# Kernel tuning notes

Measured on AMD Instinct MI355X. Metric: run time of the kernel, lower is better.

Reference implementation:

```python
import jax, jax.numpy as jnp
import numpy as np

D_MODEL = 1024
N_HEAD = 16
HEAD_DIM = D_MODEL // N_HEAD
ROPE_BASE = 10000.0


def _weight_quant(w):
    # BitNet b1.58 ternary weight quant with per-tensor absmean scale (STE).
    scale = jnp.clip(jnp.mean(jnp.abs(w)), 1e-5, None)
    wq = jnp.clip(jnp.round(w / scale), -1.0, 1.0) * scale
    return w + jax.lax.stop_gradient(wq - w)


def _act_quant(x):
    # Per-token int8 absmax activation quant (STE).
    scale = 127.0 / jnp.clip(jnp.max(jnp.abs(x), axis=-1, keepdims=True), 1e-5, None)
    xq = jnp.clip(jnp.round(x * scale), -128.0, 127.0) / scale
    return x + jax.lax.stop_gradient(xq - x)


def _bitlinear(x, w):
    # y = act_quant(x) @ weight_quant(w).T   (torch Linear convention, no bias)
    return _act_quant(x) @ _weight_quant(w).T


def _rope(x, pos):
    # x: [B, H, T, D]; half-split rotation.
    d = x.shape[-1]
    inv_freq = 1.0 / (ROPE_BASE ** (jnp.arange(0, d, 2, dtype=jnp.float32) / d))
    ang = pos[:, None].astype(jnp.float32) * inv_freq[None, :]  # [T, D/2]
    cos, sin = jnp.cos(ang), jnp.sin(ang)
    x1, x2 = x[..., : d // 2], x[..., d // 2 :]
    return jnp.concatenate([x1 * cos - x2 * sin, x1 * sin + x2 * cos], axis=-1)


def setup_inputs() -> dict:
    key = jax.random.key(0)
    k0, k1, k2, k3, k4 = jax.random.split(key, 5)
    B, T = 2, 2048
    s = 1.0 / np.sqrt(D_MODEL)
    return {
        "x": jax.random.normal(k0, (B, T, D_MODEL), dtype=jnp.float32),
        "Wq": jax.random.normal(k1, (D_MODEL, D_MODEL), dtype=jnp.float32) * s,
        "Wk": jax.random.normal(k2, (D_MODEL, D_MODEL), dtype=jnp.float32) * s,
        "Wv": jax.random.normal(k3, (D_MODEL, D_MODEL), dtype=jnp.float32) * s,
        "Wo": jax.random.normal(k4, (D_MODEL, D_MODEL), dtype=jnp.float32) * s,
    }


def reference(x, Wq, Wk, Wv, Wo):
    B, T, C = x.shape
    pos = jnp.arange(T)
    def heads(y):
        return y.reshape(B, T, N_HEAD, HEAD_DIM).transpose(0, 2, 1, 3)  # [B,H,T,D]
    q = _rope(heads(_bitlinear(x, Wq)), pos)
    k = _rope(heads(_bitlinear(x, Wk)), pos)
    v = heads(_bitlinear(x, Wv))
    scores = jnp.einsum("bhqd,bhkd->bhqk", q, k) / jnp.sqrt(jnp.float32(HEAD_DIM))
    causal = jnp.tril(jnp.ones((T, T), dtype=bool))
    scores = jnp.where(causal[None, None], scores, jnp.finfo(scores.dtype).min)
    att = jax.nn.softmax(scores, axis=-1)
    y = jnp.einsum("bhqk,bhkd->bhqd", att, v)  # [B,H,T,D]
    y = y.transpose(0, 2, 1, 3).reshape(B, T, C)
    return _bitlinear(y, Wo)
```

## Files before the change

### kernel.cpp

```cpp
#include <hip/hip_runtime.h>
#include <hip/hip_bf16.h>
#include <math.h>

typedef __bf16 bf16_t;
typedef signed char i8_t;
typedef __attribute__((ext_vector_type(8))) __bf16 bf16x8;
typedef __attribute__((ext_vector_type(4))) __bf16 bf16x4;
typedef __attribute__((ext_vector_type(4))) float f32x4;
typedef __attribute__((ext_vector_type(4))) int i32x4;

typedef __attribute__((address_space(3))) void lds_void_t;
typedef const __attribute__((address_space(1))) void glb_void_t;
#define GLOAD_LDS(g, l) __builtin_amdgcn_global_load_lds((glb_void_t*)(g), (lds_void_t*)(l), 16, 0, 0)

#define MFMA16(a,b,c) __builtin_amdgcn_mfma_f32_16x16x32_bf16(a,b,c,0,0,0)
#define MFMAI8(a,b,c) __builtin_amdgcn_mfma_i32_16x16x64_i8(a,b,c,0,0,0)

#if __has_builtin(__builtin_amdgcn_exp2f)
#define EXP2F(x) __builtin_amdgcn_exp2f(x)
#else
#define EXP2F(x) exp2f(x)
#endif

static constexpr int TSEQ = 2048;
static constexpr int CDIM = 1024;
#define NEG_BIG (-1.0e30f)
#define Q_PRESCALE 0.18033688011112042f
#define ROPE_C 0.41524101190971284f

__global__ __launch_bounds__(256) void wreduce(const float* __restrict__ W0, const float* __restrict__ W1,
                                               const float* __restrict__ W2, const float* __restrict__ W3,
                                               double* __restrict__ partial) {
  int w = blockIdx.x >> 6, b = blockIdx.x & 63;
  const float* W = (w==0)?W0:(w==1)?W1:(w==2)?W2:W3;
  const float* base = W + (size_t)b * 16384;
  double s = 0.0;
  for (int i = threadIdx.x * 4; i < 16384; i += 1024) {
    float4 v = *(const float4*)(base + i);
    s += (double)fabsf(v.x) + (double)fabsf(v.y) + (double)fabsf(v.z) + (double)fabsf(v.w);
  }
  #pragma unroll
  for (int off = 1; off < 64; off <<= 1) s += __shfl_xor(s, off);
  __shared__ double red[4];
  if ((threadIdx.x & 63) == 0) red[threadIdx.x >> 6] = s;
  __syncthreads();
  if (threadIdx.x == 0) partial[blockIdx.x] = red[0] + red[1] + red[2] + red[3];
}

__global__ __launch_bounds__(256) void prep(const float* __restrict__ W0, const float* __restrict__ W1,
                                            const float* __restrict__ W2, const float* __restrict__ W3,
                                            const double* __restrict__ partial, float* __restrict__ wscale,
                                            i8_t* __restrict__ wq_all,
                                            const float* __restrict__ xg, i8_t* __restrict__ xqg,
                                            float* __restrict__ rowfac, float2* __restrict__ ropetab) {
  int bid = blockIdx.x;
  if (bid < 4096) {
    int w = bid >> 10;
    double ssum = 0.0;
    for (int i = 0; i < 64; ++i) ssum += partial[w * 64 + i];
    float s = fmaxf((float)(ssum * (1.0 / 1048576.0)), 1e-5f);
    if ((bid & 1023) == 0 && threadIdx.x == 0) wscale[w] = s;
    const float* W = (w==0)?W0:(w==1)?W1:(w==2)?W2:W3;
    int off = ((bid & 1023) * 256 + threadIdx.x) * 4;
    float4 v = *(const float4*)(W + off);
    char4 q;
    q.x = (i8_t)(int)fminf(fmaxf(rintf(v.x / s), -1.f), 1.f);
    q.y = (i8_t)(int)fminf(fmaxf(rintf(v.y / s), -1.f), 1.f);
    q.z = (i8_t)(int)fminf(fmaxf(rintf(v.z / s), -1.f), 1.f);
    q.w = (i8_t)(int)fminf(fmaxf(rintf(v.w / s), -1.f), 1.f);
    *(char4*)(wq_all + (size_t)w * 1048576 + off) = q;
  } else if (bid < 8192) {
    int r = bid - 4096;
    float4 v = *(const float4*)(xg + (size_t)r * 1024 + threadIdx.x * 4);
    float mx = fmaxf(fmaxf(fabsf(v.x), fabsf(v.y)), fmaxf(fabsf(v.z), fabsf(v.w)));
    #pragma unroll
    for (int off = 1; off < 64; off <<= 1) mx = fmaxf(mx, __shfl_xor(mx, off));
    __shared__ float red[4];
    if ((threadIdx.x & 63) == 0) red[threadIdx.x >> 6] = mx;
    __syncthreads();
    mx = fmaxf(fmaxf(red[0], red[1]), fmaxf(red[2], red[3]));
    mx = fmaxf(mx, 1e-5f);
    float scale = 127.0f / mx;
    if (threadIdx.x == 0) rowfac[r] = mx * (1.0f / 127.0f);
    char4 q;
    q.x = (i8_t)(int)fminf(fmaxf(rintf(v.x * scale), -128.f), 127.f);
    q.y = (i8_t)(int)fminf(fmaxf(rintf(v.y * scale), -128.f), 127.f);
    q.z = (i8_t)(int)fminf(fmaxf(rintf(v.z * scale), -128.f), 127.f);
    q.w = (i8_t)(int)fminf(fmaxf(rintf(v.w * scale), -128.f), 127.f);
    *(char4*)(xqg + (size_t)r * 1024 + threadIdx.x * 4) = q;
  } else {
    int t = (bid - 8192) * 8 + (threadIdx.x >> 5);
    int ii = threadIdx.x & 31;
    float ang = (float)t * exp2f(-(float)ii * ROPE_C);
    float sn, cs;
    sincosf(ang, &sn, &cs);
    ropetab[t * 32 + ii] = make_float2(cs, sn);
  }
}

__global__ __launch_bounds__(256) void actquant(const float* __restrict__ yf0, const float* __restrict__ yf1,
                                                const float* __restrict__ den0, const float* __restrict__ den1,
                                                i8_t* __restrict__ xqg, float* __restrict__ rowfac) {
  int r = blockIdx.x;
  int b = r >> 11, t = r & 2047;
  int h = threadIdx.x >> 4;
  size_t idx = (size_t)r * 1024 + threadIdx.x * 4;
  float4 v0 = *(const float4*)(yf0 + idx);
  float4 v1 = *(const float4*)(yf1 + idx);
  size_t di = (size_t)(b * 16 + h) * 2048 + t;
  float inv = 1.0f / (den0[di] + den1[di]);
  float4 v;
  v.x = (v0.x + v1.x) * inv;
  v.y = (v0.y + v1.y) * inv;
  v.z = (v0.z + v1.z) * inv;
  v.w = (v0.w + v1.w) * inv;
  float mx = fmaxf(fmaxf(fabsf(v.x), fabsf(v.y)), fmaxf(fabsf(v.z), fabsf(v.w)));
  #pragma unroll
  for (int off = 1; off < 64; off <<= 1) mx = fmaxf(mx, __shfl_xor(mx, off));
  __shared__ float red[4];
  if ((threadIdx.x & 63) == 0) red[threadIdx.x >> 6] = mx;
  __syncthreads();
  mx = fmaxf(fmaxf(red[0], red[1]), fmaxf(red[2], red[3]));
  mx = fmaxf(mx, 1e-5f);
  float scale = 127.0f / mx;
  if (threadIdx.x == 0) rowfac[r] = mx * (1.0f / 127.0f);
  char4 q;
  q.x = (i8_t)(int)fminf(fmaxf(rintf(v.x * scale), -128.f), 127.f);
  q.y = (i8_t)(int)fminf(fmaxf(rintf(v.y * scale), -128.f), 127.f);
  q.z = (i8_t)(int)fminf(fmaxf(rintf(v.z * scale), -128.f), 127.f);
  q.w = (i8_t)(int)fminf(fmaxf(rintf(v.w * scale), -128.f), 127.f);
  *(char4*)(xqg + (size_t)r * 1024 + threadIdx.x * 4) = q;
}

__global__ __launch_bounds__(256) void gemm_qkv(const i8_t* __restrict__ xq, const i8_t* __restrict__ wq_all,
                                                const float* __restrict__ wscale, const float* __restrict__ rowfac,
                                                const float2* __restrict__ ropetab,
                                                bf16_t* __restrict__ qb, bf16_t* __restrict__ kb,
                                                bf16_t* __restrict__ vtb) {
  const int z = blockIdx.z;
  const i8_t* Bw = wq_all + (size_t)z * 1048576;
  const int m0 = blockIdx.x * 128, n0 = blockIdx.y * 128;
  const int tid = threadIdx.x;
  const int wave = tid >> 6, lane = tid & 63, quad = lane >> 4, l16 = lane & 15;
  const int wm = wave >> 1, wn = wave & 1;
  __shared__ __align__(16) i8_t As[2][128 * 64];
  __shared__ __align__(16) i8_t Bs[2][128 * 64];
  i32x4 zero = {0, 0, 0, 0};
  i32x4 acc[4][4];
  #pragma unroll
  for (int i = 0; i < 4; ++i)
    #pragma unroll
    for (int j = 0; j < 4; ++j) acc[i][j] = zero;

  const int row_s = tid >> 2;
  const int cg16 = (((tid & 3) - (row_s >> 1)) & 3) * 16;
  const int sw16 = ((quad + (l16 >> 1)) & 3) * 16;

  #pragma unroll
  for (int v2 = 0; v2 < 2; ++v2) {
    int v = tid + v2 * 256;
    int row = row_s + v2 * 64;
    GLOAD_LDS(&xq[(size_t)(m0 + row) * 1024 + cg16], &As[0][v * 16]);
    GLOAD_LDS(&Bw[(size_t)(n0 + row) * 1024 + cg16], &Bs[0][v * 16]);
  }
  __syncthreads();

  #pragma unroll 2
  for (int kt = 0; kt < 16; ++kt) {
    const int cur = kt & 1;
    if (kt < 15) {
      #pragma unroll
      for (int v2 = 0; v2 < 2; ++v2) {
        int v = tid + v2 * 256;
        int row = row_s + v2 * 64;
        GLOAD_LDS(&xq[(size_t)(m0 + row) * 1024 + (kt + 1) * 64 + cg16], &As[cur ^ 1][v * 16]);
        GLOAD_LDS(&Bw[(size_t)(n0 + row) * 1024 + (kt + 1) * 64 + cg16], &Bs[cur ^ 1][v * 16]);
      }
    }
    i32x4 af[4], bfr[4];
    #pragma unroll
    for (int i = 0; i < 4; ++i) af[i] = *(const i32x4*)&As[cur][(wm * 64 + i * 16 + l16) * 64 + sw16];
    #pragma unroll
    for (int j = 0; j < 4; ++j) bfr[j] = *(const i32x4*)&Bs[cur][(wn * 64 + j * 16 + l16) * 64 + sw16];
    if (z == 2) {
      #pragma unroll
      for (int i = 0; i < 4; ++i)
        #pragma unroll
        for (int j = 0; j < 4; ++j) acc[i][j] = MFMAI8(bfr[i], af[j], acc[i][j]);
    } else {
      #pragma unroll
      for (int i = 0; i < 4; ++i)
        #pragma unroll
        for (int j = 0; j < 4; ++j) acc[i][j] = MFMAI8(af[i], bfr[j], acc[i][j]);
    }
    __syncthreads();
  }
  float ws = wscale[z] * (z == 0 ? Q_PRESCALE : 1.0f);
  if (z <= 1) {
    bf16_t* dst = (z == 0) ? qb : kb;
    const int h = (n0 >> 6) + wn;
    #pragma unroll
    for (int i = 0; i < 4; ++i) {
      #pragma unroll
      for (int r = 0; r < 4; ++r) {
        int m = m0 + wm * 64 + i * 16 + quad * 4 + r;
        float rf = rowfac[m] * ws;
        int b = m >> 11, t = m & 2047;
        bf16_t* drow = dst + (((size_t)b * 16 + h) * 2048 + t) * 64;
        #pragma unroll
        for (int j = 0; j < 2; ++j) {
          int dd1 = j * 16 + l16;
          float2 cs2 = ropetab[t * 32 + dd1];
          float v1 = (float)acc[i][j][r] * rf;
          float v2 = (float)acc[i][j + 2][r] * rf;
          drow[dd1]      = (bf16_t)(v1 * cs2.x - v2 * cs2.y);
          drow[dd1 + 32] = (bf16_t)(v1 * cs2.y + v2 * cs2.x);
        }
      }
    }
  } else {
    const int b = m0 >> 11;
    const int tbase = (m0 & 2047) + wm * 64;
    float rfj[4];
    #pragma unroll
    for (int j = 0; j < 4; ++j) rfj[j] = rowfac[m0 + wm * 64 + j * 16 + l16] * ws;
    #pragma unroll
    for (int i = 0; i < 4; ++i) {
      #pragma unroll
      for (int r = 0; r < 4; ++r) {
        int nrow = n0 + wn * 64 + i * 16 + quad * 4 + r;
        int h = nrow >> 6, dd = nrow & 63;
        bf16_t* vrow = vtb + (((size_t)b * 16 + h) * 64 + dd) * 2048 + tbase;
        #pragma unroll
        for (int j = 0; j < 4; ++j) vrow[j * 16 + l16] = (bf16_t)((float)acc[i][j][r] * rfj[j]);
      }
    }
  }
}

__global__ __launch_bounds__(256) void gemm_out(const i8_t* __restrict__ yq, const i8_t* __restrict__ wo,
                                                const float* __restrict__ wscale, const float* __restrict__ rowfac,
                                                float* __restrict__ out) {
  const int m0 = blockIdx.x * 128, n0 = blockIdx.y * 128;
  const int tid = threadIdx.x;
  const int wave = tid >> 6, lane = tid & 63, quad = lane >> 4, l16 = lane & 15;
  const int wm = wave >> 1, wn = wave & 1;
  __shared__ __align__(16) i8_t As[2][128 * 64];
  __shared__ __align__(16) i8_t Bs[2][128 * 64];
  i32x4 zero = {0, 0, 0, 0};
  i32x4 acc[4][4];
  #pragma unroll
  for (int i = 0; i < 4; ++i)
    #pragma unroll
    for (int j = 0; j < 4; ++j) acc[i][j] = zero;

  const int row_s = tid >> 2;
  const int cg16 = (((tid & 3) - (row_s >> 1)) & 3) * 16;
  const int sw16 = ((quad + (l16 >> 1)) & 3) * 16;

  #pragma unroll
  for (int v2 = 0; v2 < 2; ++v2) {
    int v = tid + v2 * 256;
    int row = row_s + v2 * 64;
    GLOAD_LDS(&yq[(size_t)(m0 + row) * 1024 + cg16], &As[0][v * 16]);
    GLOAD_LDS(&wo[(size_t)(n0 + row) * 1024 + cg16], &Bs[0][v * 16]);
  }
  __syncthreads();

  #pragma unroll 2
  for (int kt = 0; kt < 16; ++kt) {
    const int cur = kt & 1;
    if (kt < 15) {
      #pragma unroll
      for (int v2 = 0; v2 < 2; ++v2) {
        int v = tid + v2 * 256;
        int row = row_s + v2 * 64;
        GLOAD_LDS(&yq[(size_t)(m0 + row) * 1024 + (kt + 1) * 64 + cg16], &As[cur ^ 1][v * 16]);
        GLOAD_LDS(&wo[(size_t)(n0 + row) * 1024 + (kt + 1) * 64 + cg16], &Bs[cur ^ 1][v * 16]);
      }
    }
    i32x4 af[4], bfr[4];
    #pragma unroll
    for (int i = 0; i < 4; ++i) af[i] = *(const i32x4*)&As[cur][(wm * 64 + i * 16 + l16) * 64 + sw16];
    #pragma unroll
    for (int j = 0; j < 4; ++j) bfr[j] = *(const i32x4*)&Bs[cur][(wn * 64 + j * 16 + l16) * 64 + sw16];
    #pragma unroll
    for (int i = 0; i < 4; ++i)
      #pragma unroll
      for (int j = 0; j < 4; ++j) acc[i][j] = MFMAI8(af[i], bfr[j], acc[i][j]);
    __syncthreads();
  }
  float ws = wscale[3];
  #pragma unroll
  for (int i = 0; i < 4; ++i) {
    #pragma unroll
    for (int r = 0; r < 4; ++r) {
      int m = m0 + wm * 64 + i * 16 + quad * 4 + r;
      float rf = rowfac[m] * ws;
      #pragma unroll
      for (int j = 0; j < 4; ++j) {
        int n = n0 + wn * 64 + j * 16 + l16;
        out[(size_t)m * 1024 + n] = (float)acc[i][j][r] * rf;
      }
    }
  }
}

__global__ __launch_bounds__(512) void flash_attn(const bf16_t* __restrict__ qg, const bf16_t* __restrict__ kg,
                                                  const bf16_t* __restrict__ vtg,
                                                  float* __restrict__ yf0, float* __restrict__ yf1,
                                                  float* __restrict__ den0, float* __restrict__ den1) {
  const int lid = (int)blockIdx.y * 8 + (int)blockIdx.x;
  const int par = (lid >> 3) & 1;
  const int p   = (lid >> 4) & 7;
  const int bh  = (lid & 7) * 4 + (lid >> 7);
  float* __restrict__ yo = par ? yf1 : yf0;
  float* __restrict__ dn = par ? den1 : den0;
  const int tid = threadIdx.x;
  const int wave = tid >> 6, lane = tid & 63;
  const int quad = lane >> 4, l16 = lane & 15;

  __shared__ __align__(16) bf16_t Kb[2][64 * 64];
  __shared__ __align__(16) bf16_t Vb[2][64 * 64];
  __shared__ __align__(16) bf16_t Pl[8][16 * 72];

  const int b = bh >> 4, h = bh & 15;
  bf16_t* Pw = &Pl[wave][0];

  const int r0 = tid >> 3, cblk = tid & 7;
  const int ldsOff0 = r0 * 64 + ((cblk ^ (r0 & 7)) * 8);
  const size_t bhbase = (size_t)bh * 131072;
  const bf16_t* kbase0 = kg + bhbase + r0 * 64 + cblk * 8;
  const bf16_t* vbase0 = vtg + bhbase + r0 * 2048 + cblk * 8;

  int kf_off[4][2];
  #pragma unroll
  for (int n = 0; n < 4; ++n)
    #pragma unroll
    for (int c = 0; c < 2; ++c)
      kf_off[n][c] = (n * 16 + l16) * 64 + (((c * 4 + quad) ^ (l16 & 7)) * 8);

  bf16x8 ones;
  #pragma unroll
  for (int j = 0; j < 8; ++j) ones[j] = (bf16_t)1.0f;
  f32x4 zero = {0.f, 0.f, 0.f, 0.f};

  bf16x8 kpre = *(const bf16x8*)(kbase0 + par * 4096);
  bf16x8 vpre = *(const bf16x8*)(vbase0 + par * 64);

  int cum = 0;
  #pragma unroll 1
  for (int tsel = 0; tsel < 2; ++tsel) {
    const int qt = tsel ? (15 - p) : p;
    const int kcmax = 2 * qt + 1;
    const int qbw = qt * 128 + wave * 16;

    const bf16_t* qrowp = qg + ((size_t)bh * TSEQ + qbw + l16) * 64;
    bf16x8 aq0 = *(const bf16x8*)(qrowp + quad * 8);
    bf16x8 aq1 = *(const bf16x8*)(qrowp + 32 + quad * 8);

    f32x4 o[4], o5;
    #pragma unroll
    for (int i = 0; i < 4; ++i) o[i] = zero;
    o5 = zero;

    #pragma unroll 1
    for (int kc = par; kc <= kcmax; kc += 2, ++cum) {
      const int buf = cum & 1;
      bf16_t* Kt = &Kb[buf][0];
      bf16_t* Vt = &Vb[buf][0];
      *(bf16x8*)&Kt[ldsOff0] = kpre;
      *(bf16x8*)&Vt[ldsOff0] = vpre;
      __syncthreads();
      int nkc = (kc + 2 <= kcmax) ? (kc + 2) : ((tsel == 0) ? par : -1);
      if (nkc >= 0) {
        kpre = *(const bf16x8*)(kbase0 + nkc * 4096);
        vpre = *(const bf16x8*)(vbase0 + nkc * 64);
      }

      if (kc * 64 > qbw + 15) continue;

      f32x4 s[4];
      __builtin_amdgcn_s_setprio(1);
      #pragma unroll
      for (int n = 0; n < 4; ++n) {
        bf16x8 bk0 = *(const bf16x8*)&Kt[kf_off[n][0]];
        bf16x8 bk1 = *(const bf16x8*)&Kt[kf_off[n][1]];
        s[n] = MFMA16(aq1, bk1, MFMA16(aq0, bk0, zero));
      }
      __builtin_amdgcn_s_setprio(0);
      if (kc * 64 + 63 > qbw) {
        #pragma unroll
        for (int n = 0; n < 4; ++n)
          #pragma unroll
          for (int r = 0; r < 4; ++r) {
            int kpos = kc * 64 + n * 16 + l16;
            int qpos = qbw + quad * 4 + r;
            if (kpos > qpos) s[n][r] = NEG_BIG;
          }
      }
      #pragma unroll
      for (int n = 0; n < 4; ++n)
        #pragma unroll
        for (int r = 0; r < 4; ++r)
          Pw[(quad * 4 + r) * 72 + n * 16 + l16] = (bf16_t)EXP2F(s[n][r]);

      bf16x8 ap0 = *(const bf16x8*)&Pw[l16 * 72 + quad * 8];
      bf16x8 ap1 = *(const bf16x8*)&Pw[l16 * 72 + 32 + quad * 8];
      __builtin_amdgcn_s_setprio(1);
      #pragma unroll
      for (int nh = 0; nh < 4; ++nh) {
        bf16x8 bv0 = *(const bf16x8*)&Vt[kf_off[nh][0]];
        bf16x8 bv1 = *(const bf16x8*)&Vt[kf_off[nh][1]];
        o[nh] = MFMA16(ap1, bv1, MFMA16(ap0, bv0, o[nh]));
      }
      o5 = MFMA16(ap1, ones, MFMA16(ap0, ones, o5));
      __builtin_amdgcn_s_setprio(0);
    }

    #pragma unroll
    for (int r = 0; r < 4; ++r) {
      int t = qbw + quad * 4 + r;
      float* yrow = yo + ((size_t)b * TSEQ + t) * CDIM + h * 64;
      #pragma unroll
      for (int nh = 0; nh < 4; ++nh) yrow[nh * 16 + l16] = o[nh][r];
      if (l16 == 0) dn[(size_t)bh * TSEQ + t] = o5[r];
    }
  }
}

extern "C" void kernel_launch(void* const* d_in, const int* in_sizes, int n_in,
                              void* d_out, int out_size, void* d_ws, size_t ws_size,
                              hipStream_t stream) {
  const float* x  = (const float*)d_in[0];
  const float* Wq = (const float*)d_in[1];
  const float* Wk = (const float*)d_in[2];
  const float* Wv = (const float*)d_in[3];
  const float* Wo = (const float*)d_in[4];
  float* out = (float*)d_out;

  char* ws = (char*)d_ws;
  double* wpartial = (double*)(ws);
  float* wscale   = (float*)(ws + 4096);
  float* rowfacx  = (float*)(ws + 8192);
  float* rowfacy  = (float*)(ws + 8192 + 16384);
  i8_t* wq_all    = (i8_t*)(ws + 65536);
  i8_t* xq        = wq_all + 4194304;
  bf16_t* qb      = (bf16_t*)(xq + 4194304);
  bf16_t* kb      = qb + 4194304;
  bf16_t* vtb     = kb + 4194304;
  float*  yf0     = (float*)(vtb + 4194304);
  float2* ropetab = (float2*)(yf0 + 4194304);
  float*  yf1     = (float*)((char*)ropetab + 524288);
  float*  den0    = (float*)((char*)yf1 + 16777216);
  float*  den1    = den0 + 65536;
  i8_t* yq        = xq;

  wreduce<<<256, 256, 0, stream>>>(Wq, Wk, Wv, Wo, wpartial);
  prep<<<8448, 256, 0, stream>>>(Wq, Wk, Wv, Wo, wpartial, wscale, wq_all, x, xq, rowfacx, ropetab);
  gemm_qkv<<<dim3(32, 8, 3), 256, 0, stream>>>(xq, wq_all, wscale, rowfacx, ropetab, qb, kb, vtb);
  flash_attn<<<dim3(8, 64), 512, 0, stream>>>(qb, kb, vtb, yf0, yf1, den0, den1);
  actquant<<<4096, 256, 0, stream>>>(yf0, yf1, den0, den1, yq, rowfacy);
  gemm_out<<<dim3(32, 8), 256, 0, stream>>>(yq, wq_all + 3 * 1048576, wscale, rowfacy, out);
}
```

Before: 172.4 us.

## Triple-buffer int8 GEMM LDS tiles with vmcnt-based waits

Both int8 GEMM kernels move from a double-buffered to a triple-buffered LDS pipeline that prefetches two k-tiles ahead. The full __syncthreads is replaced with an explicit s_waitcnt vmcnt(4) plus s_barrier, so only the oldest tile's global-to-LDS loads must land before each step. This is meant to hide more global memory latency behind the MFMA work. LDS use grows from 32KB to 48KB per block, which may lower occupancy, and correctness now relies on the hand-written waitcnt counts and on the full loop unroll.

```diff
diff --git a/kernel.cpp b/kernel.cpp
--- a/kernel.cpp
+++ b/kernel.cpp
@@ -21,6 +21,9 @@
 #else
 #define EXP2F(x) exp2f(x)
 #endif
+
+#define WAIT_VM4() asm volatile("s_waitcnt vmcnt(4)" ::: "memory")
+#define WAIT_VM0() asm volatile("s_waitcnt vmcnt(0)" ::: "memory")
 
 static constexpr int TSEQ = 2048;
 static constexpr int CDIM = 1024;
@@ -143,8 +146,8 @@
   const int tid = threadIdx.x;
   const int wave = tid >> 6, lane = tid & 63, quad = lane >> 4, l16 = lane & 15;
   const int wm = wave >> 1, wn = wave & 1;
-  __shared__ __align__(16) i8_t As[2][128 * 64];
-  __shared__ __align__(16) i8_t Bs[2][128 * 64];
+  __shared__ __align__(16) i8_t As[3][128 * 64];
+  __shared__ __align__(16) i8_t Bs[3][128 * 64];
   i32x4 zero = {0, 0, 0, 0};
   i32x4 acc[4][4];
   #pragma unroll
@@ -156,27 +159,26 @@
   const int cg16 = (((tid & 3) - (row_s >> 1)) & 3) * 16;
   const int sw16 = ((quad + (l16 >> 1)) & 3) * 16;
 
-  #pragma unroll
-  for (int v2 = 0; v2 < 2; ++v2) {
-    int v = tid + v2 * 256;
-    int row = row_s + v2 * 64;
-    GLOAD_LDS(&xq[(size_t)(m0 + row) * 1024 + cg16], &As[0][v * 16]);
-    GLOAD_LDS(&Bw[(size_t)(n0 + row) * 1024 + cg16], &Bs[0][v * 16]);
-  }
-  __syncthreads();
-
-  #pragma unroll 2
+  auto issue = [&](int kt) {
+    int buf = kt % 3;
+    #pragma unroll
+    for (int v2 = 0; v2 < 2; ++v2) {
+      int v = tid + v2 * 256;
+      int row = row_s + v2 * 64;
+      GLOAD_LDS(&xq[(size_t)(m0 + row) * 1024 + kt * 64 + cg16], &As[buf][v * 16]);
+      GLOAD_LDS(&Bw[(size_t)(n0 + row) * 1024 + kt * 64 + cg16], &Bs[buf][v * 16]);
+    }
+  };
+
+  issue(0);
+  issue(1);
+  WAIT_VM4();
+  __builtin_amdgcn_s_barrier();
+
+  #pragma unroll
   for (int kt = 0; kt < 16; ++kt) {
-    const int cur = kt & 1;
-    if (kt < 15) {
-      #pragma unroll
-      for (int v2 = 0; v2 < 2; ++v2) {
-        int v = tid + v2 * 256;
-        int row = row_s + v2 * 64;
-        GLOAD_LDS(&xq[(size_t)(m0 + row) * 1024 + (kt + 1) * 64 + cg16], &As[cur ^ 1][v * 16]);
-        GLOAD_LDS(&Bw[(size_t)(n0 + row) * 1024 + (kt + 1) * 64 + cg16], &Bs[cur ^ 1][v * 16]);
-      }
-    }
+    const int cur = kt % 3;
+    if (kt < 14) issue(kt + 2);
     i32x4 af[4], bfr[4];
     #pragma unroll
     for (int i = 0; i < 4; ++i) af[i] = *(const i32x4*)&As[cur][(wm * 64 + i * 16 + l16) * 64 + sw16];
@@ -193,7 +195,11 @@
         #pragma unroll
         for (int j = 0; j < 4; ++j) acc[i][j] = MFMAI8(af[i], bfr[j], acc[i][j]);
     }
-    __syncthreads();
+    if (kt < 15) {
+      if (kt < 14) { WAIT_VM4(); }
+      else         { WAIT_VM0(); }
+      __builtin_amdgcn_s_barrier();
+    }
   }
   float ws = wscale[z] * (z == 0 ? Q_PRESCALE : 1.0f);
   if (z <= 1) {
@@ -245,8 +251,8 @@
   const int tid = threadIdx.x;
   const int wave = tid >> 6, lane = tid & 63, quad = lane >> 4, l16 = lane & 15;
   const int wm = wave >> 1, wn = wave & 1;
-  __shared__ __align__(16) i8_t As[2][128 * 64];
-  __shared__ __align__(16) i8_t Bs[2][128 * 64];
+  __shared__ __align__(16) i8_t As[3][128 * 64];
+  __shared__ __align__(16) i8_t Bs[3][128 * 64];
   i32x4 zero = {0, 0, 0, 0};
   i32x4 acc[4][4];
   #pragma unroll
@@ -258,37 +264,40 @@
   const int cg16 = (((tid & 3) - (row_s >> 1)) & 3) * 16;
   const int sw16 = ((quad + (l16 >> 1)) & 3) * 16;
 
-  #pragma unroll
-  for (int v2 = 0; v2 < 2; ++v2) {
-    int v = tid + v2 * 256;
-    int row = row_s + v2 * 64;
-    GLOAD_LDS(&yq[(size_t)(m0 + row) * 1024 + cg16], &As[0][v * 16]);
-    GLOAD_LDS(&wo[(size_t)(n0 + row) * 1024 + cg16], &Bs[0][v * 16]);
-  }
-  __syncthreads();
-
-  #pragma unroll 2
+  auto issue = [&](int kt) {
+    int buf = kt % 3;
+    #pragma unroll
+    for (int v2 = 0; v2 < 2; ++v2) {
+      int v = tid + v2 * 256;
+      int row = row_s + v2 * 64;
+      GLOAD_LDS(&yq[(size_t)(m0 + row) * 1024 + kt * 64 + cg16], &As[buf][v * 16]);
+      GLOAD_LDS(&wo[(size_t)(n0 + row) * 1024 + kt * 64 + cg16], &Bs[buf][v * 16]);
+    }
+  };
+
+  issue(0);
+  issue(1);
+  WAIT_VM4();
+  __builtin_amdgcn_s_barrier();
+
+  #pragma unroll
   for (int kt = 0; kt < 16; ++kt) {
-    const int cur = kt & 1;
+    const int cur = kt % 3;
+    if (kt < 14) issue(kt + 2);
+    i32x4 af[4], bfr[4];
+    #pragma unroll
+    for (int i = 0; i < 4; ++i) af[i] = *(const i32x4*)&As[cur][(wm * 64 + i * 16 + l16) * 64 + sw16];
+    #pragma unroll
+    for (int j = 0; j < 4; ++j) bfr[j] = *(const i32x4*)&Bs[cur][(wn * 64 + j * 16 + l16) * 64 + sw16];
+    #pragma unroll
+    for (int i = 0; i < 4; ++i)
+      #pragma unroll
+      for (int j = 0; j < 4; ++j) acc[i][j] = MFMAI8(af[i], bfr[j], acc[i][j]);
     if (kt < 15) {
-      #pragma unroll
-      for (int v2 = 0; v2 < 2; ++v2) {
-        int v = tid + v2 * 256;
-        int row = row_s + v2 * 64;
-        GLOAD_LDS(&yq[(size_t)(m0 + row) * 1024 + (kt + 1) * 64 + cg16], &As[cur ^ 1][v * 16]);
-        GLOAD_LDS(&wo[(size_t)(n0 + row) * 1024 + (kt + 1) * 64 + cg16], &Bs[cur ^ 1][v * 16]);
-      }
-    }
-    i32x4 af[4], bfr[4];
-    #pragma unroll
-    for (int i = 0; i < 4; ++i) af[i] = *(const i32x4*)&As[cur][(wm * 64 + i * 16 + l16) * 64 + sw16];
-    #pragma unroll
-    for (int j = 0; j < 4; ++j) bfr[j] = *(const i32x4*)&Bs[cur][(wn * 64 + j * 16 + l16) * 64 + sw16];
-    #pragma unroll
-    for (int i = 0; i < 4; ++i)
-      #pragma unroll
-      for (int j = 0; j < 4; ++j) acc[i][j] = MFMAI8(af[i], bfr[j], acc[i][j]);
-    __syncthreads();
+      if (kt < 14) { WAIT_VM4(); }
+      else         { WAIT_VM0(); }
+      __builtin_amdgcn_s_barrier();
+    }
   }
   float ws = wscale[3];
   #pragma unroll
```

New measurement: 168.9 us. 2.1% less time.
